# Performance work log

Measured on AMD Instinct MI355X. Metric: run time of the kernel, lower is better.

## Reference

```python
import jax, jax.numpy as jnp
import numpy as np

TS = 4          # texture_size
S = 128         # image_size
DIST = 2.732    # neural_renderer default camera distance
EPS = 1e-9


def _grid_sample(img, grid):
    # img: (C,H,W); grid: (N,2) xy in [-1,1]. Bilinear, zero padding, align_corners=False
    C, H, W = img.shape
    x = (grid[:, 0] + 1.0) * (W * 0.5) - 0.5
    y = (grid[:, 1] + 1.0) * (H * 0.5) - 0.5
    x0 = jnp.floor(x)
    y0 = jnp.floor(y)
    tx = x - x0
    ty = y - y0

    def tap(xi, yi, w):
        valid = (xi >= 0) & (xi < W) & (yi >= 0) & (yi < H)
        xc = jnp.clip(xi, 0, W - 1).astype(jnp.int32)
        yc = jnp.clip(yi, 0, H - 1).astype(jnp.int32)
        return img[:, yc, xc] * jnp.where(valid, w, 0.0)[None]

    return (tap(x0, y0, (1 - tx) * (1 - ty)) + tap(x0 + 1, y0, tx * (1 - ty))
            + tap(x0, y0 + 1, (1 - tx) * ty) + tap(x0 + 1, y0 + 1, tx * ty))


def _look_at(v, eye):
    up = jnp.array([0.0, 1.0, 0.0], dtype=v.dtype)
    z = -eye / jnp.linalg.norm(eye)          # at = origin
    x = jnp.cross(up, z)
    x = x / jnp.linalg.norm(x)
    y = jnp.cross(z, x)
    y = y / jnp.linalg.norm(y)
    R = jnp.stack([x, y, z])                 # (3,3) rows = camera axes
    return (v - eye) @ R.T


def _forward(vertices, texture_image, texture_grid, faces, azi, ele):
    F = faces.shape[0]
    # --- texture resample (F.grid_sample) ---
    cols = _grid_sample(texture_image[0], texture_grid.reshape(-1, 2))  # (3, F*TS^3)
    textures = cols.T.reshape(F, TS, TS, TS, 3)

    # --- camera (orthographic look_at from elevation/azimuth, degrees) ---
    a = jnp.deg2rad(jnp.float32(azi))
    e = jnp.deg2rad(jnp.float32(ele))
    eye = DIST * jnp.stack([jnp.cos(e) * jnp.sin(a), jnp.sin(e), -jnp.cos(e) * jnp.cos(a)])
    v = _look_at(vertices, eye)              # (V,3)
    fv = v[faces]                            # (F,3,3)

    p0, p1, p2 = fv[:, 0, :2], fv[:, 1, :2], fv[:, 2, :2]
    e1 = p1 - p0
    e2 = p2 - p0
    det = e1[:, 0] * e2[:, 1] - e1[:, 1] * e2[:, 0]              # (F,)
    inv = 1.0 / jnp.where(jnp.abs(det) > EPS, det, 1.0)

    # pixel centers in NDC; row 0 = top (y=+1)
    xs = (jnp.arange(S) + 0.5) / S * 2.0 - 1.0
    ys = 1.0 - (jnp.arange(S) + 0.5) / S * 2.0
    px, py = jnp.meshgrid(xs, ys)            # (S,S)
    pix = jnp.stack([px.ravel(), py.ravel()], -1)                # (P,2), P=S*S

    d = pix[:, None, :] - p0[None]                               # (P,F,2)
    w1 = (d[..., 0] * e2[:, 1] - d[..., 1] * e2[:, 0]) * inv     # (P,F)
    w2 = (e1[:, 0] * d[..., 1] - e1[:, 1] * d[..., 0]) * inv
    w0 = 1.0 - w1 - w2
    inside = (w0 >= 0) & (w1 >= 0) & (w2 >= 0) & (jnp.abs(det) > EPS)[None]

    z = fv[:, :, 2]                                              # (F,3)
    depth = w0 * z[:, 0] + w1 * z[:, 1] + w2 * z[:, 2]
    depth = jnp.where(inside, depth, jnp.inf)
    fid = jnp.argmin(depth, axis=1)                              # (P,) nearest face (z-buffer)
    hit = jnp.isfinite(jnp.min(depth, axis=1))

    P = pix.shape[0]
    rows = jnp.arange(P)
    wb = jnp.stack([w0[rows, fid], w1[rows, fid], w2[rows, fid]], -1)   # (P,3) barycentrics
    idx = jnp.clip(jnp.floor(wb * TS).astype(jnp.int32), 0, TS - 1)     # nearest cell in TS^3 cube
    col = textures[fid, idx[:, 0], idx[:, 1], idx[:, 2]]                # (P,3)
    col = jnp.where(hit[:, None], col, 0.0)                             # black background

    img = col.reshape(S, S, 3).transpose(2, 0, 1)[None]                 # (1,3,S,S)
    return img[:, :, :, ::-1]                                           # torch.flip(images,[3])


def setup_inputs() -> dict:
    key = jax.random.key(0)
    k1, k2, k3, k4 = jax.random.split(key, 4)
    vertices = jax.random.uniform(k1, (1200, 3), minval=-0.9, maxval=0.9, dtype=jnp.float32)
    faces = jax.random.randint(k2, (2000, 3), 0, 1200, dtype=jnp.int32)
    texture_image = jax.random.uniform(k3, (1, 3, 512, 512), dtype=jnp.float32)
    texture_grid = jax.random.uniform(k4, (1, 2000 * TS ** 3, 2), minval=-1.0, maxval=1.0, dtype=jnp.float32)
    return {"vertices": vertices, "texture_image": texture_image,
            "texture_grid": texture_grid, "faces": faces, "azi": 180, "ele": 0}


def reference(vertices, texture_image, texture_grid, faces, azi, ele):
    return _forward(vertices, texture_image, texture_grid, faces, azi, ele)
```

## Files before the change

### kernel.cpp

```cpp
#include <hip/hip_runtime.h>
#include <math.h>

#define TS 4
#define SDIM 128
#define PIX (SDIM * SDIM)
#define TEXW 512
#define TEXH 512
#define EPS 1e-9f
#define NCHUNK 32
#define NTILE 64
#define MAXCF 128
#define BBOX_MARGIN 1e-3f

__device__ inline void cross3(const float a[3], const float b[3], float o[3]) {
    o[0] = a[1] * b[2] - a[2] * b[1];
    o[1] = a[2] * b[0] - a[0] * b[2];
    o[2] = a[0] * b[1] - a[1] * b[0];
}

__global__ void setup_kernel(const float* __restrict__ verts,
                             const int* __restrict__ faces,
                             const void* __restrict__ azi_p,
                             const void* __restrict__ ele_p,
                             float4* __restrict__ fd,
                             unsigned long long* __restrict__ zbuf,
                             int F, int faceBlocks) {
#pragma clang fp contract(off)
    if ((int)blockIdx.x >= faceBlocks) {
        int t = (blockIdx.x - faceBlocks) * 256 + threadIdx.x;
        if (t < PIX) zbuf[t] = ~0ull;
        return;
    }
    int f = blockIdx.x * 256 + threadIdx.x;
    if (f >= F) return;
    int ai = *(const int*)azi_p;
    float az = (ai > -360000 && ai < 360000) ? (float)ai : *(const float*)azi_p;
    int ei = *(const int*)ele_p;
    float el = (ei > -360000 && ei < 360000) ? (float)ei : *(const float*)ele_p;
    float a = az * (float)(M_PI / 180.0);
    float e = el * (float)(M_PI / 180.0);
    float ca = cosf(a), sa = sinf(a);
    float ce = cosf(e), se = sinf(e);
    float eye[3];
    eye[0] = 2.732f * (ce * sa);
    eye[1] = 2.732f * se;
    eye[2] = 2.732f * ((-ce) * ca);
    float nrm = sqrtf(eye[0] * eye[0] + eye[1] * eye[1] + eye[2] * eye[2]);
    float zv[3] = { (-eye[0]) / nrm, (-eye[1]) / nrm, (-eye[2]) / nrm };
    float up[3] = { 0.0f, 1.0f, 0.0f };
    float xv[3];
    cross3(up, zv, xv);
    float xn = sqrtf(xv[0] * xv[0] + xv[1] * xv[1] + xv[2] * xv[2]);
    xv[0] /= xn; xv[1] /= xn; xv[2] /= xn;
    float yv[3];
    cross3(zv, xv, yv);
    float yn = sqrtf(yv[0] * yv[0] + yv[1] * yv[1] + yv[2] * yv[2]);
    yv[0] /= yn; yv[1] /= yn; yv[2] /= yn;

    float q[3][3];
    for (int k = 0; k < 3; ++k) {
        int vi = faces[f * 3 + k];
        float d0 = verts[vi * 3 + 0] - eye[0];
        float d1 = verts[vi * 3 + 1] - eye[1];
        float d2 = verts[vi * 3 + 2] - eye[2];
        q[k][0] = d0 * xv[0] + d1 * xv[1] + d2 * xv[2];
        q[k][1] = d0 * yv[0] + d1 * yv[1] + d2 * yv[2];
        q[k][2] = d0 * zv[0] + d1 * zv[1] + d2 * zv[2];
    }
    float e1x = q[1][0] - q[0][0], e1y = q[1][1] - q[0][1];
    float e2x = q[2][0] - q[0][0], e2y = q[2][1] - q[0][1];
    float det = e1x * e2y - e1y * e2x;
    bool valid = fabsf(det) > EPS;
    float inv = 1.0f / (valid ? det : 1.0f);
    float z0 = valid ? q[0][2] : INFINITY;
    float z1 = valid ? q[1][2] : INFINITY;
    float z2 = valid ? q[2][2] : INFINITY;
    fd[f * 3 + 0] = make_float4(q[0][0], q[0][1], e1x, e1y);
    fd[f * 3 + 1] = make_float4(e2x, e2y, inv, 0.0f);
    fd[f * 3 + 2] = make_float4(z0, z1, z2, 0.0f);
}

__device__ inline unsigned int enc_depth(float d) {
    unsigned int u = __float_as_uint(d);
    return (u & 0x80000000u) ? ~u : (u | 0x80000000u);
}

__global__ void raster_kernel(const float4* __restrict__ fd, int F,
                              int chunkFaces,
                              unsigned long long* __restrict__ zbuf) {
#pragma clang fp contract(off)
    __shared__ float4 sA[MAXCF];
    __shared__ float4 sB[MAXCF];
    __shared__ float4 sZ[MAXCF];
    __shared__ int cnt;
    if (threadIdx.x == 0) cnt = 0;
    __syncthreads();

    int tileX = blockIdx.x & 7, tileY = blockIdx.x >> 3;
    int f0 = blockIdx.y * chunkFaces;
    float xlo = (tileX * 16 + 0.5f) / 64.0f - 1.0f - BBOX_MARGIN;
    float xhi = (tileX * 16 + 15.5f) / 64.0f - 1.0f + BBOX_MARGIN;
    float yhi = 1.0f - (tileY * 16 + 0.5f) / 64.0f + BBOX_MARGIN;
    float ylo = 1.0f - (tileY * 16 + 15.5f) / 64.0f - BBOX_MARGIN;

    int k = threadIdx.x;
    int f = f0 + k;
    if (k < chunkFaces && f < F) {
        float4 A = fd[f * 3 + 0];
        float4 B = fd[f * 3 + 1];
        float4 C = fd[f * 3 + 2];
        float p1x = A.x + A.z, p1y = A.y + A.w;
        float p2x = A.x + B.x, p2y = A.y + B.y;
        float bxmin = fminf(A.x, fminf(p1x, p2x));
        float bxmax = fmaxf(A.x, fmaxf(p1x, p2x));
        float bymin = fminf(A.y, fminf(p1y, p2y));
        float bymax = fmaxf(A.y, fmaxf(p1y, p2y));
        if (bxmin <= xhi && bxmax >= xlo && bymin <= yhi && bymax >= ylo) {
            int pos = atomicAdd(&cnt, 1);
            B.w = __int_as_float(f);
            sA[pos] = A;
            sB[pos] = B;
            sZ[pos] = C;
        }
    }
    __syncthreads();
    int n = cnt;
    if (n == 0) return;

    int j = tileX * 16 + (threadIdx.x & 15);
    int i = tileY * 16 + (threadIdx.x >> 4);
    float px = ((j + 0.5f) / 128.0f) * 2.0f - 1.0f;
    float py = 1.0f - ((i + 0.5f) / 128.0f) * 2.0f;
    float best = INFINITY;
    int bfid = 0x7fffffff;
    bool have = false;
    for (int s = 0; s < n; ++s) {
        float4 A = sA[s];
        float4 B = sB[s];
        float4 C = sZ[s];
        float dx = px - A.x, dy = py - A.y;
        float w1 = (dx * B.y - dy * B.x) * B.z;
        float w2 = (A.z * dy - A.w * dx) * B.z;
        float w0 = 1.0f - w1 - w2;
        bool inside = (w0 >= 0.0f) && (w1 >= 0.0f) && (w2 >= 0.0f);
        float depth = w0 * C.x + w1 * C.y + w2 * C.z;
        int fid = __float_as_int(B.w);
        if (inside && depth < INFINITY &&
            (depth < best || (depth == best && fid < bfid))) {
            best = depth;
            bfid = fid;
            have = true;
        }
    }
    if (have) {
        unsigned long long pack =
            ((unsigned long long)enc_depth(best) << 32) | (unsigned int)bfid;
        atomicMin(&zbuf[i * SDIM + j], pack);
    }
}

__global__ void shade_kernel(const unsigned long long* __restrict__ zbuf,
                             const float4* __restrict__ fd,
                             const float* __restrict__ img,
                             const float* __restrict__ grid,
                             float* __restrict__ out) {
#pragma clang fp contract(off)
    int t = blockIdx.x * 256 + threadIdx.x;
    int i = t >> 7, j = t & 127;
    int o = i * SDIM + (SDIM - 1 - j);
    unsigned long long pack = zbuf[t];
    if (pack == ~0ull) {
        out[0 * PIX + o] = 0.0f;
        out[1 * PIX + o] = 0.0f;
        out[2 * PIX + o] = 0.0f;
        return;
    }
    int bfid = (int)(unsigned int)(pack & 0xffffffffu);
    float4 A = fd[bfid * 3 + 0];
    float4 B = fd[bfid * 3 + 1];
    float px = ((j + 0.5f) / 128.0f) * 2.0f - 1.0f;
    float py = 1.0f - ((i + 0.5f) / 128.0f) * 2.0f;
    float dx = px - A.x, dy = py - A.y;
    float w1 = (dx * B.y - dy * B.x) * B.z;
    float w2 = (A.z * dy - A.w * dx) * B.z;
    float w0 = 1.0f - w1 - w2;
    int i0 = min(max((int)floorf(w0 * (float)TS), 0), TS - 1);
    int i1 = min(max((int)floorf(w1 * (float)TS), 0), TS - 1);
    int i2 = min(max((int)floorf(w2 * (float)TS), 0), TS - 1);
    int sidx = bfid * (TS * TS * TS) + i0 * 16 + i1 * 4 + i2;
    float gx = grid[2 * sidx], gy = grid[2 * sidx + 1];
    float x = (gx + 1.0f) * (TEXW * 0.5f) - 0.5f;
    float y = (gy + 1.0f) * (TEXH * 0.5f) - 0.5f;
    float x0f = floorf(x), y0f = floorf(y);
    float tx = x - x0f, ty = y - y0f;
    int x0 = (int)x0f, y0 = (int)y0f;
    float w00 = (1.0f - tx) * (1.0f - ty);
    float w10 = tx * (1.0f - ty);
    float w01 = (1.0f - tx) * ty;
    float w11 = tx * ty;
    bool vx0 = (x0 >= 0) && (x0 < TEXW);
    bool vx1 = (x0 + 1 >= 0) && (x0 + 1 < TEXW);
    bool vy0 = (y0 >= 0) && (y0 < TEXH);
    bool vy1 = (y0 + 1 >= 0) && (y0 + 1 < TEXH);
    int xc0 = min(max(x0, 0), TEXW - 1);
    int xc1 = min(max(x0 + 1, 0), TEXW - 1);
    int yc0 = min(max(y0, 0), TEXH - 1);
    int yc1 = min(max(y0 + 1, 0), TEXH - 1);
    float W00 = (vx0 && vy0) ? w00 : 0.0f;
    float W10 = (vx1 && vy0) ? w10 : 0.0f;
    float W01 = (vx0 && vy1) ? w01 : 0.0f;
    float W11 = (vx1 && vy1) ? w11 : 0.0f;
    for (int c = 0; c < 3; ++c) {
        const float* ic = img + c * (TEXH * TEXW);
        float acc = ic[yc0 * TEXW + xc0] * W00;
        acc = acc + ic[yc0 * TEXW + xc1] * W10;
        acc = acc + ic[yc1 * TEXW + xc0] * W01;
        acc = acc + ic[yc1 * TEXW + xc1] * W11;
        out[c * PIX + o] = acc;
    }
}

extern "C" void kernel_launch(void* const* d_in, const int* in_sizes, int n_in,
                              void* d_out, int out_size, void* d_ws,
                              size_t ws_size, hipStream_t stream) {
    const float* verts = (const float*)d_in[0];
    const float* img = (const float*)d_in[1];
    const float* grid = (const float*)d_in[2];
    const int* faces = (const int*)d_in[3];
    const void* azi = d_in[4];
    const void* ele = d_in[5];
    float* out = (float*)d_out;

    int F = in_sizes[3] / 3;

    char* ws = (char*)d_ws;
    size_t off = 0;
    float4* fd = (float4*)(ws + off);
    off += ((size_t)F * 3 * 16 + 255) & ~(size_t)255;
    unsigned long long* zbuf = (unsigned long long*)(ws + off);

    int faceBlocks = (F + 255) / 256;
    int zBlocks = (PIX + 255) / 256;
    int chunkFaces = (F + NCHUNK - 1) / NCHUNK;

    setup_kernel<<<faceBlocks + zBlocks, 256, 0, stream>>>(
        verts, faces, azi, ele, fd, zbuf, F, faceBlocks);
    raster_kernel<<<dim3(NTILE, NCHUNK), 256, 0, stream>>>(fd, F, chunkFaces,
                                                           zbuf);
    shade_kernel<<<PIX / 256, 256, 0, stream>>>(zbuf, fd, img, grid, out);
}
```

Baseline: 86.22 us.

## Fuse setup, raster and shade into one cooperative kernel with grid syncs

Replaces the three separate launches (setup, raster, shade) with a single cooperative kernel that uses grid-wide syncs between phases, removing two kernel launch gaps. The face chunk count is halved (16 chunks of up to 125 faces), so there are fewer blocks and fewer atomicMin contenders, and the per-tile face buffer grows to 192 with an overflow guard. In exchange, grid.sync has its own cost, launch_bounds are added, and the result depends on all 1024 blocks being co-resident, which a cooperative launch requires.

```diff
diff --git a/kernel.cpp b/kernel.cpp
--- a/kernel.cpp
+++ b/kernel.cpp
@@ -1,5 +1,8 @@
 #include <hip/hip_runtime.h>
+#include <hip/hip_cooperative_groups.h>
 #include <math.h>
+
+namespace cg = cooperative_groups;
 
 #define TS 4
 #define SDIM 128
@@ -7,216 +10,220 @@
 #define TEXW 512
 #define TEXH 512
 #define EPS 1e-9f
-#define NCHUNK 32
+#define NCHUNK 16
 #define NTILE 64
-#define MAXCF 128
+#define NBLOCK (NTILE * NCHUNK)
+#define MAXCF 192
 #define BBOX_MARGIN 1e-3f
 
-__device__ inline void cross3(const float a[3], const float b[3], float o[3]) {
-    o[0] = a[1] * b[2] - a[2] * b[1];
-    o[1] = a[2] * b[0] - a[0] * b[2];
-    o[2] = a[0] * b[1] - a[1] * b[0];
-}
-
-__global__ void setup_kernel(const float* __restrict__ verts,
-                             const int* __restrict__ faces,
-                             const void* __restrict__ azi_p,
-                             const void* __restrict__ ele_p,
-                             float4* __restrict__ fd,
-                             unsigned long long* __restrict__ zbuf,
-                             int F, int faceBlocks) {
-#pragma clang fp contract(off)
-    if ((int)blockIdx.x >= faceBlocks) {
-        int t = (blockIdx.x - faceBlocks) * 256 + threadIdx.x;
-        if (t < PIX) zbuf[t] = ~0ull;
-        return;
-    }
-    int f = blockIdx.x * 256 + threadIdx.x;
-    if (f >= F) return;
-    int ai = *(const int*)azi_p;
-    float az = (ai > -360000 && ai < 360000) ? (float)ai : *(const float*)azi_p;
-    int ei = *(const int*)ele_p;
-    float el = (ei > -360000 && ei < 360000) ? (float)ei : *(const float*)ele_p;
-    float a = az * (float)(M_PI / 180.0);
-    float e = el * (float)(M_PI / 180.0);
-    float ca = cosf(a), sa = sinf(a);
-    float ce = cosf(e), se = sinf(e);
-    float eye[3];
-    eye[0] = 2.732f * (ce * sa);
-    eye[1] = 2.732f * se;
-    eye[2] = 2.732f * ((-ce) * ca);
-    float nrm = sqrtf(eye[0] * eye[0] + eye[1] * eye[1] + eye[2] * eye[2]);
-    float zv[3] = { (-eye[0]) / nrm, (-eye[1]) / nrm, (-eye[2]) / nrm };
-    float up[3] = { 0.0f, 1.0f, 0.0f };
-    float xv[3];
-    cross3(up, zv, xv);
-    float xn = sqrtf(xv[0] * xv[0] + xv[1] * xv[1] + xv[2] * xv[2]);
-    xv[0] /= xn; xv[1] /= xn; xv[2] /= xn;
-    float yv[3];
-    cross3(zv, xv, yv);
-    float yn = sqrtf(yv[0] * yv[0] + yv[1] * yv[1] + yv[2] * yv[2]);
-    yv[0] /= yn; yv[1] /= yn; yv[2] /= yn;
-
-    float q[3][3];
-    for (int k = 0; k < 3; ++k) {
-        int vi = faces[f * 3 + k];
-        float d0 = verts[vi * 3 + 0] - eye[0];
-        float d1 = verts[vi * 3 + 1] - eye[1];
-        float d2 = verts[vi * 3 + 2] - eye[2];
-        q[k][0] = d0 * xv[0] + d1 * xv[1] + d2 * xv[2];
-        q[k][1] = d0 * yv[0] + d1 * yv[1] + d2 * yv[2];
-        q[k][2] = d0 * zv[0] + d1 * zv[1] + d2 * zv[2];
-    }
-    float e1x = q[1][0] - q[0][0], e1y = q[1][1] - q[0][1];
-    float e2x = q[2][0] - q[0][0], e2y = q[2][1] - q[0][1];
-    float det = e1x * e2y - e1y * e2x;
-    bool valid = fabsf(det) > EPS;
-    float inv = 1.0f / (valid ? det : 1.0f);
-    float z0 = valid ? q[0][2] : INFINITY;
-    float z1 = valid ? q[1][2] : INFINITY;
-    float z2 = valid ? q[2][2] : INFINITY;
-    fd[f * 3 + 0] = make_float4(q[0][0], q[0][1], e1x, e1y);
-    fd[f * 3 + 1] = make_float4(e2x, e2y, inv, 0.0f);
-    fd[f * 3 + 2] = make_float4(z0, z1, z2, 0.0f);
-}
-
-__device__ inline unsigned int enc_depth(float d) {
+__device__ __forceinline__ unsigned int enc_depth(float d) {
     unsigned int u = __float_as_uint(d);
     return (u & 0x80000000u) ? ~u : (u | 0x80000000u);
 }
 
-__global__ void raster_kernel(const float4* __restrict__ fd, int F,
-                              int chunkFaces,
-                              unsigned long long* __restrict__ zbuf) {
+__global__ __launch_bounds__(256, 4) void fused_kernel(
+    const float* __restrict__ verts, const int* __restrict__ faces,
+    const void* __restrict__ azi_p, const void* __restrict__ ele_p,
+    const float* __restrict__ img, const float* __restrict__ grid,
+    float4* __restrict__ fd, unsigned long long* __restrict__ zbuf,
+    float* __restrict__ out, int F, int chunkFaces) {
 #pragma clang fp contract(off)
-    __shared__ float4 sA[MAXCF];
-    __shared__ float4 sB[MAXCF];
-    __shared__ float4 sZ[MAXCF];
-    __shared__ int cnt;
-    if (threadIdx.x == 0) cnt = 0;
-    __syncthreads();
-
-    int tileX = blockIdx.x & 7, tileY = blockIdx.x >> 3;
-    int f0 = blockIdx.y * chunkFaces;
-    float xlo = (tileX * 16 + 0.5f) / 64.0f - 1.0f - BBOX_MARGIN;
-    float xhi = (tileX * 16 + 15.5f) / 64.0f - 1.0f + BBOX_MARGIN;
-    float yhi = 1.0f - (tileY * 16 + 0.5f) / 64.0f + BBOX_MARGIN;
-    float ylo = 1.0f - (tileY * 16 + 15.5f) / 64.0f - BBOX_MARGIN;
-
-    int k = threadIdx.x;
-    int f = f0 + k;
-    if (k < chunkFaces && f < F) {
-        float4 A = fd[f * 3 + 0];
-        float4 B = fd[f * 3 + 1];
-        float4 C = fd[f * 3 + 2];
-        float p1x = A.x + A.z, p1y = A.y + A.w;
-        float p2x = A.x + B.x, p2y = A.y + B.y;
-        float bxmin = fminf(A.x, fminf(p1x, p2x));
-        float bxmax = fmaxf(A.x, fmaxf(p1x, p2x));
-        float bymin = fminf(A.y, fminf(p1y, p2y));
-        float bymax = fmaxf(A.y, fmaxf(p1y, p2y));
-        if (bxmin <= xhi && bxmax >= xlo && bymin <= yhi && bymax >= ylo) {
-            int pos = atomicAdd(&cnt, 1);
-            B.w = __int_as_float(f);
-            sA[pos] = A;
-            sB[pos] = B;
-            sZ[pos] = C;
+    cg::grid_group gg = cg::this_grid();
+
+    {
+        int t = blockIdx.x * 256 + threadIdx.x;
+        if (t < F) {
+            int f = t;
+            int ai = *(const int*)azi_p;
+            float az = (ai > -360000 && ai < 360000) ? (float)ai
+                                                     : *(const float*)azi_p;
+            int ei = *(const int*)ele_p;
+            float el = (ei > -360000 && ei < 360000) ? (float)ei
+                                                     : *(const float*)ele_p;
+            float a = az * (float)(M_PI / 180.0);
+            float e = el * (float)(M_PI / 180.0);
+            float ca = cosf(a), sa = sinf(a);
+            float ce = cosf(e), se = sinf(e);
+            float eye[3];
+            eye[0] = 2.732f * (ce * sa);
+            eye[1] = 2.732f * se;
+            eye[2] = 2.732f * ((-ce) * ca);
+            float nrm =
+                sqrtf(eye[0] * eye[0] + eye[1] * eye[1] + eye[2] * eye[2]);
+            float zv[3] = { (-eye[0]) / nrm, (-eye[1]) / nrm,
+                            (-eye[2]) / nrm };
+            float cx0 = 1.0f * zv[2] - 0.0f * zv[1];
+            float cx1 = 0.0f * zv[0] - 0.0f * zv[2];
+            float cx2 = 0.0f * zv[1] - 1.0f * zv[0];
+            float xn = sqrtf(cx0 * cx0 + cx1 * cx1 + cx2 * cx2);
+            float xv[3] = { cx0 / xn, cx1 / xn, cx2 / xn };
+            float cy0 = zv[1] * xv[2] - zv[2] * xv[1];
+            float cy1 = zv[2] * xv[0] - zv[0] * xv[2];
+            float cy2 = zv[0] * xv[1] - zv[1] * xv[0];
+            float yn = sqrtf(cy0 * cy0 + cy1 * cy1 + cy2 * cy2);
+            float yv[3] = { cy0 / yn, cy1 / yn, cy2 / yn };
+
+            float q[3][3];
+            for (int k = 0; k < 3; ++k) {
+                int vi = faces[f * 3 + k];
+                float d0 = verts[vi * 3 + 0] - eye[0];
+                float d1 = verts[vi * 3 + 1] - eye[1];
+                float d2 = verts[vi * 3 + 2] - eye[2];
+                q[k][0] = d0 * xv[0] + d1 * xv[1] + d2 * xv[2];
+                q[k][1] = d0 * yv[0] + d1 * yv[1] + d2 * yv[2];
+                q[k][2] = d0 * zv[0] + d1 * zv[1] + d2 * zv[2];
+            }
+            float e1x = q[1][0] - q[0][0], e1y = q[1][1] - q[0][1];
+            float e2x = q[2][0] - q[0][0], e2y = q[2][1] - q[0][1];
+            float det = e1x * e2y - e1y * e2x;
+            bool valid = fabsf(det) > EPS;
+            float inv = 1.0f / (valid ? det : 1.0f);
+            float z0 = valid ? q[0][2] : INFINITY;
+            float z1 = valid ? q[1][2] : INFINITY;
+            float z2 = valid ? q[2][2] : INFINITY;
+            fd[f * 3 + 0] = make_float4(q[0][0], q[0][1], e1x, e1y);
+            fd[f * 3 + 1] = make_float4(e2x, e2y, inv, 0.0f);
+            fd[f * 3 + 2] = make_float4(z0, z1, z2, 0.0f);
+        } else if (t < F + PIX) {
+            zbuf[t - F] = ~0ull;
         }
     }
-    __syncthreads();
-    int n = cnt;
-    if (n == 0) return;
-
-    int j = tileX * 16 + (threadIdx.x & 15);
-    int i = tileY * 16 + (threadIdx.x >> 4);
-    float px = ((j + 0.5f) / 128.0f) * 2.0f - 1.0f;
-    float py = 1.0f - ((i + 0.5f) / 128.0f) * 2.0f;
-    float best = INFINITY;
-    int bfid = 0x7fffffff;
-    bool have = false;
-    for (int s = 0; s < n; ++s) {
-        float4 A = sA[s];
-        float4 B = sB[s];
-        float4 C = sZ[s];
+    gg.sync();
+
+    {
+        __shared__ float4 sA[MAXCF];
+        __shared__ float4 sB[MAXCF];
+        __shared__ float4 sZ[MAXCF];
+        __shared__ int cnt;
+        if (threadIdx.x == 0) cnt = 0;
+        __syncthreads();
+
+        int tile = blockIdx.x & (NTILE - 1);
+        int chunk = blockIdx.x >> 6;
+        int tileX = tile & 7, tileY = tile >> 3;
+        int f0 = chunk * chunkFaces;
+        float xlo = (tileX * 16 + 0.5f) / 64.0f - 1.0f - BBOX_MARGIN;
+        float xhi = (tileX * 16 + 15.5f) / 64.0f - 1.0f + BBOX_MARGIN;
+        float yhi = 1.0f - (tileY * 16 + 0.5f) / 64.0f + BBOX_MARGIN;
+        float ylo = 1.0f - (tileY * 16 + 15.5f) / 64.0f - BBOX_MARGIN;
+
+        for (int k = threadIdx.x; k < chunkFaces; k += 256) {
+            int f = f0 + k;
+            if (f < F) {
+                float4 A = fd[f * 3 + 0];
+                float4 B = fd[f * 3 + 1];
+                float4 C = fd[f * 3 + 2];
+                float p1x = A.x + A.z, p1y = A.y + A.w;
+                float p2x = A.x + B.x, p2y = A.y + B.y;
+                float bxmin = fminf(A.x, fminf(p1x, p2x));
+                float bxmax = fmaxf(A.x, fmaxf(p1x, p2x));
+                float bymin = fminf(A.y, fminf(p1y, p2y));
+                float bymax = fmaxf(A.y, fmaxf(p1y, p2y));
+                if (bxmin <= xhi && bxmax >= xlo && bymin <= yhi &&
+                    bymax >= ylo) {
+                    int pos = atomicAdd(&cnt, 1);
+                    if (pos < MAXCF) {
+                        B.w = __int_as_float(f);
+                        sA[pos] = A;
+                        sB[pos] = B;
+                        sZ[pos] = C;
+                    }
+                }
+            }
+        }
+        __syncthreads();
+        int n = min(cnt, MAXCF);
+
+        if (n > 0) {
+            int j = tileX * 16 + (threadIdx.x & 15);
+            int i = tileY * 16 + (threadIdx.x >> 4);
+            float px = ((j + 0.5f) / 128.0f) * 2.0f - 1.0f;
+            float py = 1.0f - ((i + 0.5f) / 128.0f) * 2.0f;
+            float best = INFINITY;
+            int bfid = 0x7fffffff;
+            bool have = false;
+            for (int s = 0; s < n; ++s) {
+                float4 A = sA[s];
+                float4 B = sB[s];
+                float4 C = sZ[s];
+                float dx = px - A.x, dy = py - A.y;
+                float w1 = (dx * B.y - dy * B.x) * B.z;
+                float w2 = (A.z * dy - A.w * dx) * B.z;
+                float w0 = 1.0f - w1 - w2;
+                bool inside = (w0 >= 0.0f) && (w1 >= 0.0f) && (w2 >= 0.0f);
+                float depth = w0 * C.x + w1 * C.y + w2 * C.z;
+                int fid = __float_as_int(B.w);
+                if (inside && depth < INFINITY &&
+                    (depth < best || (depth == best && fid < bfid))) {
+                    best = depth;
+                    bfid = fid;
+                    have = true;
+                }
+            }
+            if (have) {
+                unsigned long long pack =
+                    ((unsigned long long)enc_depth(best) << 32) |
+                    (unsigned int)bfid;
+                atomicMin(&zbuf[i * SDIM + j], pack);
+            }
+        }
+    }
+    gg.sync();
+
+    if (blockIdx.x < PIX / 256) {
+        int t = blockIdx.x * 256 + threadIdx.x;
+        int i = t >> 7, j = t & 127;
+        int o = i * SDIM + (SDIM - 1 - j);
+        unsigned long long pack = zbuf[t];
+        if (pack == ~0ull) {
+            out[0 * PIX + o] = 0.0f;
+            out[1 * PIX + o] = 0.0f;
+            out[2 * PIX + o] = 0.0f;
+            return;
+        }
+        int bfid = (int)(unsigned int)(pack & 0xffffffffu);
+        float4 A = fd[bfid * 3 + 0];
+        float4 B = fd[bfid * 3 + 1];
+        float px = ((j + 0.5f) / 128.0f) * 2.0f - 1.0f;
+        float py = 1.0f - ((i + 0.5f) / 128.0f) * 2.0f;
         float dx = px - A.x, dy = py - A.y;
         float w1 = (dx * B.y - dy * B.x) * B.z;
         float w2 = (A.z * dy - A.w * dx) * B.z;
         float w0 = 1.0f - w1 - w2;
-        bool inside = (w0 >= 0.0f) && (w1 >= 0.0f) && (w2 >= 0.0f);
-        float depth = w0 * C.x + w1 * C.y + w2 * C.z;
-        int fid = __float_as_int(B.w);
-        if (inside && depth < INFINITY &&
-            (depth < best || (depth == best && fid < bfid))) {
-            best = depth;
-            bfid = fid;
-            have = true;
-        }
-    }
-    if (have) {
-        unsigned long long pack =
-            ((unsigned long long)enc_depth(best) << 32) | (unsigned int)bfid;
-        atomicMin(&zbuf[i * SDIM + j], pack);
-    }
-}
-
-__global__ void shade_kernel(const unsigned long long* __restrict__ zbuf,
-                             const float4* __restrict__ fd,
-                             const float* __restrict__ img,
-                             const float* __restrict__ grid,
-                             float* __restrict__ out) {
-#pragma clang fp contract(off)
-    int t = blockIdx.x * 256 + threadIdx.x;
-    int i = t >> 7, j = t & 127;
-    int o = i * SDIM + (SDIM - 1 - j);
-    unsigned long long pack = zbuf[t];
-    if (pack == ~0ull) {
-        out[0 * PIX + o] = 0.0f;
-        out[1 * PIX + o] = 0.0f;
-        out[2 * PIX + o] = 0.0f;
-        return;
-    }
-    int bfid = (int)(unsigned int)(pack & 0xffffffffu);
-    float4 A = fd[bfid * 3 + 0];
-    float4 B = fd[bfid * 3 + 1];
-    float px = ((j + 0.5f) / 128.0f) * 2.0f - 1.0f;
-    float py = 1.0f - ((i + 0.5f) / 128.0f) * 2.0f;
-    float dx = px - A.x, dy = py - A.y;
-    float w1 = (dx * B.y - dy * B.x) * B.z;
-    float w2 = (A.z * dy - A.w * dx) * B.z;
-    float w0 = 1.0f - w1 - w2;
-    int i0 = min(max((int)floorf(w0 * (float)TS), 0), TS - 1);
-    int i1 = min(max((int)floorf(w1 * (float)TS), 0), TS - 1);
-    int i2 = min(max((int)floorf(w2 * (float)TS), 0), TS - 1);
-    int sidx = bfid * (TS * TS * TS) + i0 * 16 + i1 * 4 + i2;
-    float gx = grid[2 * sidx], gy = grid[2 * sidx + 1];
-    float x = (gx + 1.0f) * (TEXW * 0.5f) - 0.5f;
-    float y = (gy + 1.0f) * (TEXH * 0.5f) - 0.5f;
-    float x0f = floorf(x), y0f = floorf(y);
-    float tx = x - x0f, ty = y - y0f;
-    int x0 = (int)x0f, y0 = (int)y0f;
-    float w00 = (1.0f - tx) * (1.0f - ty);
-    float w10 = tx * (1.0f - ty);
-    float w01 = (1.0f - tx) * ty;
-    float w11 = tx * ty;
-    bool vx0 = (x0 >= 0) && (x0 < TEXW);
-    bool vx1 = (x0 + 1 >= 0) && (x0 + 1 < TEXW);
-    bool vy0 = (y0 >= 0) && (y0 < TEXH);
-    bool vy1 = (y0 + 1 >= 0) && (y0 + 1 < TEXH);
-    int xc0 = min(max(x0, 0), TEXW - 1);
-    int xc1 = min(max(x0 + 1, 0), TEXW - 1);
-    int yc0 = min(max(y0, 0), TEXH - 1);
-    int yc1 = min(max(y0 + 1, 0), TEXH - 1);
-    float W00 = (vx0 && vy0) ? w00 : 0.0f;
-    float W10 = (vx1 && vy0) ? w10 : 0.0f;
-    float W01 = (vx0 && vy1) ? w01 : 0.0f;
-    float W11 = (vx1 && vy1) ? w11 : 0.0f;
-    for (int c = 0; c < 3; ++c) {
-        const float* ic = img + c * (TEXH * TEXW);
-        float acc = ic[yc0 * TEXW + xc0] * W00;
-        acc = acc + ic[yc0 * TEXW + xc1] * W10;
-        acc = acc + ic[yc1 * TEXW + xc0] * W01;
-        acc = acc + ic[yc1 * TEXW + xc1] * W11;
-        out[c * PIX + o] = acc;
+        int i0 = min(max((int)floorf(w0 * (float)TS), 0), TS - 1);
+        int i1 = min(max((int)floorf(w1 * (float)TS), 0), TS - 1);
+        int i2 = min(max((int)floorf(w2 * (float)TS), 0), TS - 1);
+        int sidx = bfid * (TS * TS * TS) + i0 * 16 + i1 * 4 + i2;
+        float gx = grid[2 * sidx], gy = grid[2 * sidx + 1];
+        float x = (gx + 1.0f) * (TEXW * 0.5f) - 0.5f;
+        float y = (gy + 1.0f) * (TEXH * 0.5f) - 0.5f;
+        float x0f = floorf(x), y0f = floorf(y);
+        float tx = x - x0f, ty = y - y0f;
+        int x0 = (int)x0f, y0 = (int)y0f;
+        float w00 = (1.0f - tx) * (1.0f - ty);
+        float w10 = tx * (1.0f - ty);
+        float w01 = (1.0f - tx) * ty;
+        float w11 = tx * ty;
+        bool vx0 = (x0 >= 0) && (x0 < TEXW);
+        bool vx1 = (x0 + 1 >= 0) && (x0 + 1 < TEXW);
+        bool vy0 = (y0 >= 0) && (y0 < TEXH);
+        bool vy1 = (y0 + 1 >= 0) && (y0 + 1 < TEXH);
+        int xc0 = min(max(x0, 0), TEXW - 1);
+        int xc1 = min(max(x0 + 1, 0), TEXW - 1);
+        int yc0 = min(max(y0, 0), TEXH - 1);
+        int yc1 = min(max(y0 + 1, 0), TEXH - 1);
+        float W00 = (vx0 && vy0) ? w00 : 0.0f;
+        float W10 = (vx1 && vy0) ? w10 : 0.0f;
+        float W01 = (vx0 && vy1) ? w01 : 0.0f;
+        float W11 = (vx1 && vy1) ? w11 : 0.0f;
+        for (int c = 0; c < 3; ++c) {
+            const float* ic = img + c * (TEXH * TEXW);
+            float acc = ic[yc0 * TEXW + xc0] * W00;
+            acc = acc + ic[yc0 * TEXW + xc1] * W10;
+            acc = acc + ic[yc1 * TEXW + xc0] * W01;
+            acc = acc + ic[yc1 * TEXW + xc1] * W11;
+            out[c * PIX + o] = acc;
+        }
     }
 }
 
@@ -239,13 +246,11 @@
     off += ((size_t)F * 3 * 16 + 255) & ~(size_t)255;
     unsigned long long* zbuf = (unsigned long long*)(ws + off);
 
-    int faceBlocks = (F + 255) / 256;
-    int zBlocks = (PIX + 255) / 256;
     int chunkFaces = (F + NCHUNK - 1) / NCHUNK;
 
-    setup_kernel<<<faceBlocks + zBlocks, 256, 0, stream>>>(
-        verts, faces, azi, ele, fd, zbuf, F, faceBlocks);
-    raster_kernel<<<dim3(NTILE, NCHUNK), 256, 0, stream>>>(fd, F, chunkFaces,
-                                                           zbuf);
-    shade_kernel<<<PIX / 256, 256, 0, stream>>>(zbuf, fd, img, grid, out);
+    void* args[] = { (void*)&verts, (void*)&faces, (void*)&azi, (void*)&ele,
+                     (void*)&img,   (void*)&grid,  (void*)&fd,  (void*)&zbuf,
+                     (void*)&out,   (void*)&F,     (void*)&chunkFaces };
+    hipLaunchCooperativeKernel((const void*)fused_kernel, dim3(NBLOCK),
+                               dim3(256), args, 0, stream);
 }
```

New measurement: 232.9 us. 170% more time.

## Fuse raster and shade kernels using a completion-ticket grid barrier

Applied to the files above, without the earlier changes.

Merges the shade pass into the raster kernel. Every block takes a ticket from a global atomic counter after rasterizing, and the last 64 ticket holders spin until all blocks are done, then each shades one 256-pixel slice. The aim is to remove one kernel launch and the gap between launches. The cost is a spin-wait on a global atomic in the late blocks, which relies on all blocks being resident or already finished. zbuf reads go through atomics so the other blocks' writes are visible.

```diff
diff --git a/kernel.cpp b/kernel.cpp
--- a/kernel.cpp
+++ b/kernel.cpp
@@ -9,6 +9,7 @@
 #define EPS 1e-9f
 #define NCHUNK 32
 #define NTILE 64
+#define NRB (NTILE * NCHUNK)
 #define MAXCF 128
 #define BBOX_MARGIN 1e-3f
 
@@ -24,11 +25,13 @@
                              const void* __restrict__ ele_p,
                              float4* __restrict__ fd,
                              unsigned long long* __restrict__ zbuf,
+                             unsigned int* __restrict__ done,
                              int F, int faceBlocks) {
 #pragma clang fp contract(off)
     if ((int)blockIdx.x >= faceBlocks) {
         int t = (blockIdx.x - faceBlocks) * 256 + threadIdx.x;
         if (t < PIX) zbuf[t] = ~0ull;
+        if (t == 0) *done = 0u;
         return;
     }
     int f = blockIdx.x * 256 + threadIdx.x;
@@ -85,19 +88,26 @@
     return (u & 0x80000000u) ? ~u : (u | 0x80000000u);
 }
 
-__global__ void raster_kernel(const float4* __restrict__ fd, int F,
-                              int chunkFaces,
-                              unsigned long long* __restrict__ zbuf) {
+__global__ void raster_shade_kernel(const float4* __restrict__ fd, int F,
+                                    int chunkFaces,
+                                    unsigned long long* __restrict__ zbuf,
+                                    unsigned int* __restrict__ done,
+                                    const float* __restrict__ img,
+                                    const float* __restrict__ grid,
+                                    float* __restrict__ out) {
 #pragma clang fp contract(off)
     __shared__ float4 sA[MAXCF];
     __shared__ float4 sB[MAXCF];
     __shared__ float4 sZ[MAXCF];
     __shared__ int cnt;
+    __shared__ unsigned int sticket;
     if (threadIdx.x == 0) cnt = 0;
     __syncthreads();
 
-    int tileX = blockIdx.x & 7, tileY = blockIdx.x >> 3;
-    int f0 = blockIdx.y * chunkFaces;
+    int tile = blockIdx.x & (NTILE - 1);
+    int chunk = blockIdx.x >> 6;
+    int tileX = tile & 7, tileY = tile >> 3;
+    int f0 = chunk * chunkFaces;
     float xlo = (tileX * 16 + 0.5f) / 64.0f - 1.0f - BBOX_MARGIN;
     float xhi = (tileX * 16 + 15.5f) / 64.0f - 1.0f + BBOX_MARGIN;
     float yhi = 1.0f - (tileY * 16 + 0.5f) / 64.0f + BBOX_MARGIN;
@@ -125,50 +135,58 @@
     }
     __syncthreads();
     int n = cnt;
-    if (n == 0) return;
-
-    int j = tileX * 16 + (threadIdx.x & 15);
-    int i = tileY * 16 + (threadIdx.x >> 4);
-    float px = ((j + 0.5f) / 128.0f) * 2.0f - 1.0f;
-    float py = 1.0f - ((i + 0.5f) / 128.0f) * 2.0f;
-    float best = INFINITY;
-    int bfid = 0x7fffffff;
-    bool have = false;
-    for (int s = 0; s < n; ++s) {
-        float4 A = sA[s];
-        float4 B = sB[s];
-        float4 C = sZ[s];
-        float dx = px - A.x, dy = py - A.y;
-        float w1 = (dx * B.y - dy * B.x) * B.z;
-        float w2 = (A.z * dy - A.w * dx) * B.z;
-        float w0 = 1.0f - w1 - w2;
-        bool inside = (w0 >= 0.0f) && (w1 >= 0.0f) && (w2 >= 0.0f);
-        float depth = w0 * C.x + w1 * C.y + w2 * C.z;
-        int fid = __float_as_int(B.w);
-        if (inside && depth < INFINITY &&
-            (depth < best || (depth == best && fid < bfid))) {
-            best = depth;
-            bfid = fid;
-            have = true;
+
+    if (n > 0) {
+        int j = tileX * 16 + (threadIdx.x & 15);
+        int i = tileY * 16 + (threadIdx.x >> 4);
+        float px = ((j + 0.5f) / 128.0f) * 2.0f - 1.0f;
+        float py = 1.0f - ((i + 0.5f) / 128.0f) * 2.0f;
+        float best = INFINITY;
+        int bfid = 0x7fffffff;
+        bool have = false;
+        for (int s = 0; s < n; ++s) {
+            float4 A = sA[s];
+            float4 B = sB[s];
+            float4 C = sZ[s];
+            float dx = px - A.x, dy = py - A.y;
+            float w1 = (dx * B.y - dy * B.x) * B.z;
+            float w2 = (A.z * dy - A.w * dx) * B.z;
+            float w0 = 1.0f - w1 - w2;
+            bool inside = (w0 >= 0.0f) && (w1 >= 0.0f) && (w2 >= 0.0f);
+            float depth = w0 * C.x + w1 * C.y + w2 * C.z;
+            int fid = __float_as_int(B.w);
+            if (inside && depth < INFINITY &&
+                (depth < best || (depth == best && fid < bfid))) {
+                best = depth;
+                bfid = fid;
+                have = true;
+            }
         }
-    }
-    if (have) {
-        unsigned long long pack =
-            ((unsigned long long)enc_depth(best) << 32) | (unsigned int)bfid;
-        atomicMin(&zbuf[i * SDIM + j], pack);
-    }
-}
-
-__global__ void shade_kernel(const unsigned long long* __restrict__ zbuf,
-                             const float4* __restrict__ fd,
-                             const float* __restrict__ img,
-                             const float* __restrict__ grid,
-                             float* __restrict__ out) {
-#pragma clang fp contract(off)
-    int t = blockIdx.x * 256 + threadIdx.x;
+        if (have) {
+            unsigned long long pack =
+                ((unsigned long long)enc_depth(best) << 32) |
+                (unsigned int)bfid;
+            atomicMin(&zbuf[i * SDIM + j], pack);
+        }
+    }
+
+    __threadfence();
+    if (threadIdx.x == 0) sticket = atomicAdd(done, 1u) + 1u;
+    __syncthreads();
+    unsigned int ticket = sticket;
+    if (ticket <= NRB - (PIX / 256)) return;
+    int slice = (int)ticket - (NRB - (PIX / 256)) - 1;
+
+    if (threadIdx.x == 0) {
+        while (atomicAdd(done, 0u) < (unsigned int)NRB) {  }
+    }
+    __syncthreads();
+    __threadfence();
+
+    int t = slice * 256 + threadIdx.x;
     int i = t >> 7, j = t & 127;
     int o = i * SDIM + (SDIM - 1 - j);
-    unsigned long long pack = zbuf[t];
+    unsigned long long pack = atomicMin(&zbuf[t], ~0ull);
     if (pack == ~0ull) {
         out[0 * PIX + o] = 0.0f;
         out[1 * PIX + o] = 0.0f;
@@ -238,14 +256,15 @@
     float4* fd = (float4*)(ws + off);
     off += ((size_t)F * 3 * 16 + 255) & ~(size_t)255;
     unsigned long long* zbuf = (unsigned long long*)(ws + off);
+    off += (size_t)PIX * 8;
+    unsigned int* done = (unsigned int*)(ws + off);
 
     int faceBlocks = (F + 255) / 256;
     int zBlocks = (PIX + 255) / 256;
     int chunkFaces = (F + NCHUNK - 1) / NCHUNK;
 
     setup_kernel<<<faceBlocks + zBlocks, 256, 0, stream>>>(
-        verts, faces, azi, ele, fd, zbuf, F, faceBlocks);
-    raster_kernel<<<dim3(NTILE, NCHUNK), 256, 0, stream>>>(fd, F, chunkFaces,
-                                                           zbuf);
-    shade_kernel<<<PIX / 256, 256, 0, stream>>>(zbuf, fd, img, grid, out);
-}
+        verts, faces, azi, ele, fd, zbuf, done, F, faceBlocks);
+    raster_shade_kernel<<<NRB, 256, 0, stream>>>(fd, F, chunkFaces, zbuf,
+                                                 done, img, grid, out);
+}
```

After: 196.0 us. +127.3%, slower.
